# Kernel tuning notes

Measured on AMD Instinct MI355X. Metric: run time of the kernel, lower is better.

The kernel has to match this reference:

```python
import jax, jax.numpy as jnp
import numpy as np

V, D, T, H, L, NC = 50257, 1024, 512, 16, 4, 3
HS = D // H  # head size 64
DFF = 4 * D
B = 16


def _ln(x, g, b, eps=1e-5):
    mu = jnp.mean(x, axis=-1, keepdims=True)
    var = jnp.var(x, axis=-1, keepdims=True)
    return (x - mu) * jax.lax.rsqrt(var + eps) * g + b


def setup_inputs() -> dict:
    key = jax.random.key(0)
    ks = jax.random.split(key, 20)
    s = 0.02
    inp = {
        "x": jax.random.randint(ks[0], (B, T), 0, V),
        "tok_emb": jax.random.normal(ks[1], (V, D), jnp.float32) * s,
        "pos_emb": jax.random.normal(ks[2], (T, D), jnp.float32) * s,
        "Wq": jax.random.normal(ks[3], (L, H, D, HS), jnp.float32) * s,
        "Wk": jax.random.normal(ks[4], (L, H, D, HS), jnp.float32) * s,
        "Wv": jax.random.normal(ks[5], (L, H, D, HS), jnp.float32) * s,
        "Wproj": jax.random.normal(ks[6], (L, H * HS, D), jnp.float32) * s,
        "bproj": jnp.zeros((L, D), jnp.float32),
        "ln1_g": jnp.ones((L, D), jnp.float32),
        "ln1_b": jnp.zeros((L, D), jnp.float32),
        "ln2_g": jnp.ones((L, D), jnp.float32),
        "ln2_b": jnp.zeros((L, D), jnp.float32),
        "W1": jax.random.normal(ks[7], (L, D, DFF), jnp.float32) * s,
        "b1": jnp.zeros((L, DFF), jnp.float32),
        "W2": jax.random.normal(ks[8], (L, DFF, D), jnp.float32) * s,
        "b2": jnp.zeros((L, D), jnp.float32),
        "lnf_g": jnp.ones((D,), jnp.float32),
        "lnf_b": jnp.zeros((D,), jnp.float32),
        "Wout": jax.random.normal(ks[9], (T * D, NC), jnp.float32) * s,
        "bout": jnp.zeros((NC,), jnp.float32),
    }
    return inp


def reference(x, tok_emb, pos_emb, Wq, Wk, Wv, Wproj, bproj, ln1_g, ln1_b,
              ln2_g, ln2_b, W1, b1, W2, b2, lnf_g, lnf_b, Wout, bout):
    Bx, Tx = x.shape
    h = tok_emb[x] + pos_emb[:Tx]  # [B,T,D]; dropout=identity (eval)
    scale = HS ** -0.5
    for l in range(L):
        z = _ln(h, ln1_g[l], ln1_b[l])
        q = jnp.einsum('btd,hde->bhte', z, Wq[l])
        k = jnp.einsum('btd,hde->bhte', z, Wk[l])
        v = jnp.einsum('btd,hde->bhte', z, Wv[l])
        att = jax.nn.softmax(jnp.einsum('bhte,bhse->bhts', q, k) * scale, axis=-1)
        o = jnp.einsum('bhts,bhse->bhte', att, v)  # [B,H,T,HS]
        o = o.transpose(0, 2, 1, 3).reshape(Bx, Tx, H * HS)
        h = h + o @ Wproj[l] + bproj[l]
        z2 = _ln(h, ln2_g[l], ln2_b[l])
        ffn = jax.nn.gelu(z2 @ W1[l] + b1[l], approximate=False) @ W2[l] + b2[l]
        h = h + ffn
    h = _ln(h, lnf_g, lnf_b)
    logits = h.reshape(Bx, -1) @ Wout + bout  # [B,NC]
    return logits
```

## Files before the change

kernel.cpp:

```cpp
#include <hip/hip_runtime.h>
#include <math.h>
#include <stdint.h>

#define DEV __device__ __forceinline__

constexpr int Bz = 16, T = 512, D = 1024, H = 16, HS = 64, Lx = 4, DFF = 4096, NCn = 3;
constexpr int BT = Bz * T;

typedef __attribute__((ext_vector_type(8))) short v8s;
typedef __attribute__((ext_vector_type(4))) float v4f;

DEV uint16_t f2bf(float f) {
  uint32_t u = __float_as_uint(f);
  u += 0x7fff + ((u >> 16) & 1);
  return (uint16_t)(u >> 16);
}
DEV float bf2f(uint16_t v) { return __uint_as_float(((uint32_t)v) << 16); }

DEV void async_copy16(const void* g, void* l) {
  __builtin_amdgcn_global_load_lds(
      (const __attribute__((address_space(1))) uint32_t*)g,
      (__attribute__((address_space(3))) uint32_t*)l, 16, 0, 0);
}

__global__ void transpose_cast_kernel(const float* __restrict__ in, uint16_t* __restrict__ out,
                                      int R, int C) {
  __shared__ float tile[32][33];
  long bo = (long)blockIdx.z * R * C;
  in += bo; out += bo;
  int c0 = blockIdx.x * 32, r0 = blockIdx.y * 32;
  int tx = threadIdx.x, ty = threadIdx.y;
  for (int i = 0; i < 32; i += 8)
    tile[ty + i][tx] = in[(long)(r0 + ty + i) * C + (c0 + tx)];
  __syncthreads();
  for (int i = 0; i < 32; i += 8)
    out[(long)(c0 + ty + i) * R + (r0 + tx)] = f2bf(tile[tx][ty + i]);
}

__global__ void embed_kernel(const int* __restrict__ x, const float* __restrict__ tok,
                             const float* __restrict__ pos, float* __restrict__ h) {
  int row = blockIdx.x;
  int t = row & (T - 1);
  int id = x[row];
  const float4* tr = (const float4*)(tok + (long)id * D);
  const float4* pr = (const float4*)(pos + (long)t * D);
  float4* hr = (float4*)(h + (long)row * D);
  int i = threadIdx.x;
  float4 a = tr[i], b = pr[i];
  hr[i] = make_float4(a.x + b.x, a.y + b.y, a.z + b.z, a.w + b.w);
}

template <bool OUT_BF16>
__global__ void ln_kernel(const float* __restrict__ in, const float* __restrict__ g,
                          const float* __restrict__ b, void* __restrict__ out) {
  int row = blockIdx.x;
  int i = threadIdx.x;
  const float4* xr = (const float4*)(in + (long)row * D);
  float4 v = xr[i];
  float s = v.x + v.y + v.z + v.w;
  float s2 = v.x * v.x + v.y * v.y + v.z * v.z + v.w * v.w;
  for (int off = 32; off; off >>= 1) { s += __shfl_down(s, off); s2 += __shfl_down(s2, off); }
  __shared__ float sh1[4], sh2[4];
  int wid = i >> 6, lane = i & 63;
  if (lane == 0) { sh1[wid] = s; sh2[wid] = s2; }
  __syncthreads();
  s = sh1[0] + sh1[1] + sh1[2] + sh1[3];
  s2 = sh2[0] + sh2[1] + sh2[2] + sh2[3];
  float mu = s * (1.0f / D);
  float rstd = rsqrtf(s2 * (1.0f / D) - mu * mu + 1e-5f);
  float4 gv = ((const float4*)g)[i];
  float4 bv = ((const float4*)b)[i];
  float o0 = (v.x - mu) * rstd * gv.x + bv.x;
  float o1 = (v.y - mu) * rstd * gv.y + bv.y;
  float o2 = (v.z - mu) * rstd * gv.z + bv.z;
  float o3 = (v.w - mu) * rstd * gv.w + bv.w;
  if constexpr (OUT_BF16) {
    uint16_t* orow = (uint16_t*)out + (long)row * D;
    orow[4 * i + 0] = f2bf(o0); orow[4 * i + 1] = f2bf(o1);
    orow[4 * i + 2] = f2bf(o2); orow[4 * i + 3] = f2bf(o3);
  } else {
    ((float4*)((float*)out + (long)row * D))[i] = make_float4(o0, o1, o2, o3);
  }
}

__global__ void softmax_kernel(uint16_t* __restrict__ S) {
  long row = blockIdx.x;
  uint32_t* r = (uint32_t*)(S + row * (long)T);
  int i = threadIdx.x;
  uint32_t u = r[i];
  float a = __uint_as_float(u << 16) * 0.125f;
  float b = __uint_as_float(u & 0xffff0000u) * 0.125f;
  float m = fmaxf(a, b);
  for (int off = 32; off; off >>= 1) m = fmaxf(m, __shfl_down(m, off));
  __shared__ float sh[4], sh2[4];
  int wid = i >> 6, lane = i & 63;
  if (lane == 0) sh[wid] = m;
  __syncthreads();
  m = fmaxf(fmaxf(sh[0], sh[1]), fmaxf(sh[2], sh[3]));
  float ea = expf(a - m), eb = expf(b - m);
  float s = ea + eb;
  for (int off = 32; off; off >>= 1) s += __shfl_down(s, off);
  if (lane == 0) sh2[wid] = s;
  __syncthreads();
  float inv = 1.0f / (sh2[0] + sh2[1] + sh2[2] + sh2[3]);
  r[i] = (uint32_t)f2bf(ea * inv) | ((uint32_t)f2bf(eb * inv) << 16);
}

enum { MQK = 0, MVT = 1, MBF = 2, MO = 3, MRES = 4, MGELU = 5 };

template <int BM, int BN, int WGM, int WGN, int MODE>
__global__ void gemm_kernel(const uint16_t* __restrict__ A, const uint16_t* __restrict__ Bt,
                            int M, int N, int K,
                            long strideA, long strideB, long strideC,
                            const float* __restrict__ bias, void* __restrict__ Cout) {
  constexpr int BK = 32;
  constexpr int WM = BM / WGM, WN = BN / WGN;
  constexpr int TM = WM / 16, TN = WN / 16;
  __shared__ __align__(16) uint16_t As[BM * BK];
  __shared__ __align__(16) uint16_t Bs[BN * BK];
  int batch = blockIdx.z;
  A += (long)batch * strideA;
  Bt += (long)batch * strideB;
  int bn0 = blockIdx.x * BN, bm0 = blockIdx.y * BM;
  int tid = threadIdx.x, wid = tid >> 6, lane = tid & 63;
  int wm = wid / WGN, wn = wid % WGN;
  v4f acc[TM][TN] = {};
  const int laneRow = lane >> 2;
  const int laneB = (lane & 3) * 16;

  for (int k0 = 0; k0 < K; k0 += BK) {
    __syncthreads();
    for (int c = wid; c < BM / 16; c += 4) {
      int row = bm0 + c * 16 + laneRow;
      const char* g = (const char*)(A + (long)row * K + k0) + laneB;
      async_copy16(g, (char*)As + c * 1024);
    }
    for (int c = wid; c < BN / 16; c += 4) {
      int col = bn0 + c * 16 + laneRow;
      const char* g = (const char*)(Bt + (long)col * K + k0) + laneB;
      async_copy16(g, (char*)Bs + c * 1024);
    }
    __syncthreads();

    int kq = (lane >> 4) * 8;
    v8s af[TM], bfr[TN];
#pragma unroll
    for (int i = 0; i < TM; i++) {
      int r = wm * WM + i * 16 + (lane & 15);
      af[i] = *(const v8s*)&As[r * BK + kq];
    }
#pragma unroll
    for (int j = 0; j < TN; j++) {
      int c = wn * WN + j * 16 + (lane & 15);
      bfr[j] = *(const v8s*)&Bs[c * BK + kq];
    }
#pragma unroll
    for (int i = 0; i < TM; i++)
#pragma unroll
      for (int j = 0; j < TN; j++)
        acc[i][j] = __builtin_amdgcn_mfma_f32_16x16x32_bf16(af[i], bfr[j], acc[i][j], 0, 0, 0);
  }

#pragma unroll
  for (int i = 0; i < TM; i++) {
    int row0 = bm0 + wm * WM + i * 16 + (lane >> 4) * 4;
#pragma unroll
    for (int j = 0; j < TN; j++) {
      int col = bn0 + wn * WN + j * 16 + (lane & 15);
#pragma unroll
      for (int r = 0; r < 4; r++) {
        int row = row0 + r;
        float val = acc[i][j][r];
        if constexpr (MODE == MQK) {
          int b = row >> 9, t = row & 511, hh = col >> 6, e = col & 63;
          ((uint16_t*)Cout)[((long)(b * H + hh) * T + t) * HS + e] = f2bf(val);
        } else if constexpr (MODE == MVT) {
          int b = row >> 9, t = row & 511, hh = col >> 6, e = col & 63;
          ((uint16_t*)Cout)[((long)(b * H + hh) * HS + e) * T + t] = f2bf(val);
        } else if constexpr (MODE == MBF) {
          ((uint16_t*)Cout)[(long)batch * strideC + (long)row * N + col] = f2bf(val);
        } else if constexpr (MODE == MO) {
          int b = batch >> 4, hh = batch & 15;
          ((uint16_t*)Cout)[((long)(b * T + row) * H + hh) * HS + col] = f2bf(val);
        } else if constexpr (MODE == MRES) {
          ((float*)Cout)[(long)row * N + col] += val + bias[col];
        } else if constexpr (MODE == MGELU) {
          float xg = val + bias[col];
          float gl = 0.5f * xg * (1.0f + erff(xg * 0.70710678118f));
          ((uint16_t*)Cout)[(long)row * N + col] = f2bf(gl);
        }
      }
    }
  }
}

__global__ void logits_init(const float* __restrict__ bout, float* __restrict__ out) {
  int i = threadIdx.x;
  if (i < Bz * NCn) out[i] = bout[i % NCn];
}
__global__ void logits_kernel(const float* __restrict__ hf, const float* __restrict__ Wout,
                              float* __restrict__ out) {
  int b = blockIdx.y, c = blockIdx.z;
  long base = (long)blockIdx.x * 8192;
  const float* hv = hf + (long)b * T * D + base;
  const float* w = Wout + base * NCn + c;
  float s = 0.f;
  for (int i = threadIdx.x; i < 8192; i += 256) s += hv[i] * w[(long)i * NCn];
  for (int off = 32; off; off >>= 1) s += __shfl_down(s, off);
  __shared__ float sh[4];
  int wid = threadIdx.x >> 6, lane = threadIdx.x & 63;
  if (lane == 0) sh[wid] = s;
  __syncthreads();
  if (threadIdx.x == 0) atomicAdd(out + b * NCn + c, sh[0] + sh[1] + sh[2] + sh[3]);
}

extern "C" void kernel_launch(void* const* d_in, const int* in_sizes, int n_in,
                              void* d_out, int out_size, void* d_ws, size_t ws_size,
                              hipStream_t stream) {
  const int* x = (const int*)d_in[0];
  const float* tok = (const float*)d_in[1];
  const float* pos = (const float*)d_in[2];
  const float* Wq = (const float*)d_in[3];
  const float* Wk = (const float*)d_in[4];
  const float* Wv = (const float*)d_in[5];
  const float* Wproj = (const float*)d_in[6];
  const float* bproj = (const float*)d_in[7];
  const float* ln1g = (const float*)d_in[8];
  const float* ln1b = (const float*)d_in[9];
  const float* ln2g = (const float*)d_in[10];
  const float* ln2b = (const float*)d_in[11];
  const float* W1 = (const float*)d_in[12];
  const float* b1 = (const float*)d_in[13];
  const float* W2 = (const float*)d_in[14];
  const float* b2 = (const float*)d_in[15];
  const float* lnfg = (const float*)d_in[16];
  const float* lnfb = (const float*)d_in[17];
  const float* Wout = (const float*)d_in[18];
  const float* bout = (const float*)d_in[19];
  float* out = (float*)d_out;

  char* ws = (char*)d_ws;
  size_t off = 0;
  auto alloc = [&](size_t bytes) { char* p = ws + off; off += (bytes + 255) & ~(size_t)255; return p; };
  uint16_t* wqT = (uint16_t*)alloc((size_t)Lx * D * D * 2);
  uint16_t* wkT = (uint16_t*)alloc((size_t)Lx * D * D * 2);
  uint16_t* wvT = (uint16_t*)alloc((size_t)Lx * D * D * 2);
  uint16_t* wpT = (uint16_t*)alloc((size_t)Lx * D * D * 2);
  uint16_t* w1T = (uint16_t*)alloc((size_t)Lx * D * DFF * 2);
  uint16_t* w2T = (uint16_t*)alloc((size_t)Lx * D * DFF * 2);
  float* h = (float*)alloc((size_t)BT * D * 4);
  uint16_t* z = (uint16_t*)alloc((size_t)BT * D * 2);
  uint16_t* q = (uint16_t*)alloc((size_t)Bz * H * T * HS * 2);
  uint16_t* kb = (uint16_t*)alloc((size_t)Bz * H * T * HS * 2);
  uint16_t* vt = (uint16_t*)alloc((size_t)Bz * H * T * HS * 2);
  uint16_t* S = (uint16_t*)alloc((size_t)Bz * H * T * T * 2);
  uint16_t* o = (uint16_t*)alloc((size_t)BT * D * 2);
  uint16_t* a1 = (uint16_t*)alloc((size_t)BT * DFF * 2);
  (void)ws_size; (void)in_sizes; (void)n_in; (void)out_size;

  dim3 tb(32, 8);
  transpose_cast_kernel<<<dim3(HS / 32, D / 32, Lx * H), tb, 0, stream>>>(Wq, wqT, D, HS);
  transpose_cast_kernel<<<dim3(HS / 32, D / 32, Lx * H), tb, 0, stream>>>(Wk, wkT, D, HS);
  transpose_cast_kernel<<<dim3(HS / 32, D / 32, Lx * H), tb, 0, stream>>>(Wv, wvT, D, HS);
  transpose_cast_kernel<<<dim3(D / 32, D / 32, Lx), tb, 0, stream>>>(Wproj, wpT, D, D);
  transpose_cast_kernel<<<dim3(DFF / 32, D / 32, Lx), tb, 0, stream>>>(W1, w1T, D, DFF);
  transpose_cast_kernel<<<dim3(D / 32, DFF / 32, Lx), tb, 0, stream>>>(W2, w2T, DFF, D);

  embed_kernel<<<BT, 256, 0, stream>>>(x, tok, pos, h);

  for (int l = 0; l < Lx; l++) {
    const uint16_t* wq_l = wqT + (size_t)l * D * D;
    const uint16_t* wk_l = wkT + (size_t)l * D * D;
    const uint16_t* wv_l = wvT + (size_t)l * D * D;
    const uint16_t* wp_l = wpT + (size_t)l * D * D;
    const uint16_t* w1_l = w1T + (size_t)l * D * DFF;
    const uint16_t* w2_l = w2T + (size_t)l * D * DFF;

    ln_kernel<true><<<BT, 256, 0, stream>>>(h, ln1g + l * D, ln1b + l * D, z);

    gemm_kernel<128, 128, 2, 2, MQK><<<dim3(D / 128, BT / 128, 1), 256, 0, stream>>>(
        z, wq_l, BT, D, D, 0, 0, 0, nullptr, q);
    gemm_kernel<128, 128, 2, 2, MQK><<<dim3(D / 128, BT / 128, 1), 256, 0, stream>>>(
        z, wk_l, BT, D, D, 0, 0, 0, nullptr, kb);
    gemm_kernel<128, 128, 2, 2, MVT><<<dim3(D / 128, BT / 128, 1), 256, 0, stream>>>(
        z, wv_l, BT, D, D, 0, 0, 0, nullptr, vt);

    gemm_kernel<128, 128, 2, 2, MBF><<<dim3(T / 128, T / 128, Bz * H), 256, 0, stream>>>(
        q, kb, T, T, HS, (long)T * HS, (long)T * HS, (long)T * T, nullptr, S);

    softmax_kernel<<<(long)Bz * H * T, 256, 0, stream>>>(S);

    gemm_kernel<128, 64, 4, 1, MO><<<dim3(1, T / 128, Bz * H), 256, 0, stream>>>(
        S, vt, T, HS, T, (long)T * T, (long)HS * T, 0, nullptr, o);

    gemm_kernel<128, 128, 2, 2, MRES><<<dim3(D / 128, BT / 128, 1), 256, 0, stream>>>(
        o, wp_l, BT, D, D, 0, 0, 0, bproj + l * D, h);

    ln_kernel<true><<<BT, 256, 0, stream>>>(h, ln2g + l * D, ln2b + l * D, z);

    gemm_kernel<128, 128, 2, 2, MGELU><<<dim3(DFF / 128, BT / 128, 1), 256, 0, stream>>>(
        z, w1_l, BT, DFF, D, 0, 0, 0, b1 + l * DFF, a1);

    gemm_kernel<128, 128, 2, 2, MRES><<<dim3(D / 128, BT / 128, 1), 256, 0, stream>>>(
        a1, w2_l, BT, D, DFF, 0, 0, 0, b2 + l * D, h);
  }

  ln_kernel<false><<<BT, 256, 0, stream>>>(h, lnfg, lnfb, h);
  logits_init<<<1, 64, 0, stream>>>(bout, out);
  logits_kernel<<<dim3(64, Bz, NCn), 256, 0, stream>>>(h, Wout, out);
}
```

Baseline: 2.904 ms.

## Fuse QKV GEMM, swizzle LDS tiles, split-K atomics, warp-per-row softmax

Packs the Q, K and V weights into one transposed buffer so a single GEMM produces all three projections, removing two launches and rereads of the activations. An XOR swizzle is added to the LDS tile layout to reduce bank conflicts on fragment loads. The grid is reordered so blockIdx.x walks M. The residual GEMMs (projection and FFN2) are split along K into two halves that accumulate into h with atomicAdd, doubling block count at the cost of atomic traffic. Softmax is rewritten so each wavefront handles one row with 16-byte loads and shuffle reductions, dropping shared memory and block syncs.

```diff
diff --git a/kernel.cpp b/kernel.cpp
--- a/kernel.cpp
+++ b/kernel.cpp
@@ -6,6 +6,7 @@
 
 constexpr int Bz = 16, T = 512, D = 1024, H = 16, HS = 64, Lx = 4, DFF = 4096, NCn = 3;
 constexpr int BT = Bz * T;
+constexpr long QSZ = (long)Bz * H * T * HS;
 
 typedef __attribute__((ext_vector_type(8))) short v8s;
 typedef __attribute__((ext_vector_type(4))) float v4f;
@@ -15,7 +16,6 @@
   u += 0x7fff + ((u >> 16) & 1);
   return (uint16_t)(u >> 16);
 }
-DEV float bf2f(uint16_t v) { return __uint_as_float(((uint32_t)v) << 16); }
 
 DEV void async_copy16(const void* g, void* l) {
   __builtin_amdgcn_global_load_lds(
@@ -24,10 +24,11 @@
 }
 
 __global__ void transpose_cast_kernel(const float* __restrict__ in, uint16_t* __restrict__ out,
-                                      int R, int C) {
+                                      int R, int C, long s1, long s2, int zdiv) {
   __shared__ float tile[32][33];
-  long bo = (long)blockIdx.z * R * C;
-  in += bo; out += bo;
+  int zz = blockIdx.z;
+  in += (long)zz * R * C;
+  out += (long)(zz / zdiv) * s1 + (long)(zz % zdiv) * s2;
   int c0 = blockIdx.x * 32, r0 = blockIdx.y * 32;
   int tx = threadIdx.x, ty = threadIdx.y;
   for (int i = 0; i < 32; i += 8)
@@ -84,33 +85,41 @@
 }
 
 __global__ void softmax_kernel(uint16_t* __restrict__ S) {
-  long row = blockIdx.x;
-  uint32_t* r = (uint32_t*)(S + row * (long)T);
-  int i = threadIdx.x;
-  uint32_t u = r[i];
-  float a = __uint_as_float(u << 16) * 0.125f;
-  float b = __uint_as_float(u & 0xffff0000u) * 0.125f;
-  float m = fmaxf(a, b);
-  for (int off = 32; off; off >>= 1) m = fmaxf(m, __shfl_down(m, off));
-  __shared__ float sh[4], sh2[4];
-  int wid = i >> 6, lane = i & 63;
-  if (lane == 0) sh[wid] = m;
-  __syncthreads();
-  m = fmaxf(fmaxf(sh[0], sh[1]), fmaxf(sh[2], sh[3]));
-  float ea = expf(a - m), eb = expf(b - m);
-  float s = ea + eb;
-  for (int off = 32; off; off >>= 1) s += __shfl_down(s, off);
-  if (lane == 0) sh2[wid] = s;
-  __syncthreads();
-  float inv = 1.0f / (sh2[0] + sh2[1] + sh2[2] + sh2[3]);
-  r[i] = (uint32_t)f2bf(ea * inv) | ((uint32_t)f2bf(eb * inv) << 16);
-}
-
-enum { MQK = 0, MVT = 1, MBF = 2, MO = 3, MRES = 4, MGELU = 5 };
+  int wid = threadIdx.x >> 6, lane = threadIdx.x & 63;
+  long row = (long)blockIdx.x * 4 + wid;
+  uint4* p = (uint4*)(S + row * T) + lane;
+  uint4 u = *p;
+  uint32_t w[4] = {u.x, u.y, u.z, u.w};
+  float lo[4], hi[4];
+  float m = -1e30f;
+#pragma unroll
+  for (int i = 0; i < 4; i++) {
+    lo[i] = __uint_as_float(w[i] << 16) * 0.125f;
+    hi[i] = __uint_as_float(w[i] & 0xffff0000u) * 0.125f;
+    m = fmaxf(m, fmaxf(lo[i], hi[i]));
+  }
+  for (int off = 32; off; off >>= 1) m = fmaxf(m, __shfl_xor(m, off));
+  float s = 0.f;
+#pragma unroll
+  for (int i = 0; i < 4; i++) {
+    lo[i] = expf(lo[i] - m); hi[i] = expf(hi[i] - m);
+    s += lo[i] + hi[i];
+  }
+  for (int off = 32; off; off >>= 1) s += __shfl_xor(s, off);
+  float inv = 1.0f / s;
+  uint4 o;
+  uint32_t* ow = (uint32_t*)&o;
+#pragma unroll
+  for (int i = 0; i < 4; i++)
+    ow[i] = (uint32_t)f2bf(lo[i] * inv) | ((uint32_t)f2bf(hi[i] * inv) << 16);
+  *p = o;
+}
+
+enum { MQKV = 0, MBF = 1, MO = 2, MATOMIC = 3, MGELU = 4 };
 
 template <int BM, int BN, int WGM, int WGN, int MODE>
 __global__ void gemm_kernel(const uint16_t* __restrict__ A, const uint16_t* __restrict__ Bt,
-                            int M, int N, int K,
+                            int M, int N, int K, int lda, int ldb,
                             long strideA, long strideB, long strideC,
                             const float* __restrict__ bias, void* __restrict__ Cout) {
   constexpr int BK = 32;
@@ -118,42 +127,40 @@
   constexpr int TM = WM / 16, TN = WN / 16;
   __shared__ __align__(16) uint16_t As[BM * BK];
   __shared__ __align__(16) uint16_t Bs[BN * BK];
-  int batch = blockIdx.z;
+  int kz = 0, batch = 0;
+  if constexpr (MODE == MATOMIC) kz = blockIdx.z; else batch = blockIdx.z;
   A += (long)batch * strideA;
   Bt += (long)batch * strideB;
-  int bn0 = blockIdx.x * BN, bm0 = blockIdx.y * BM;
+  const int kb0 = kz * K;
+  int bm0 = blockIdx.x * BM, bn0 = blockIdx.y * BN;
   int tid = threadIdx.x, wid = tid >> 6, lane = tid & 63;
   int wm = wid / WGN, wn = wid % WGN;
   v4f acc[TM][TN] = {};
+
   const int laneRow = lane >> 2;
-  const int laneB = (lane & 3) * 16;
-
-  for (int k0 = 0; k0 < K; k0 += BK) {
+  const int laneB = ((lane & 3) ^ ((laneRow >> 1) & 3)) * 16;
+  const int rl = lane & 15;
+  const int cx16 = (rl * 4 + ((lane >> 4) ^ ((rl >> 1) & 3))) * 16;
+
+  for (int k0 = kb0; k0 < kb0 + K; k0 += BK) {
     __syncthreads();
     for (int c = wid; c < BM / 16; c += 4) {
       int row = bm0 + c * 16 + laneRow;
-      const char* g = (const char*)(A + (long)row * K + k0) + laneB;
-      async_copy16(g, (char*)As + c * 1024);
+      async_copy16((const char*)(A + (long)row * lda + k0) + laneB, (char*)As + c * 1024);
     }
     for (int c = wid; c < BN / 16; c += 4) {
       int col = bn0 + c * 16 + laneRow;
-      const char* g = (const char*)(Bt + (long)col * K + k0) + laneB;
-      async_copy16(g, (char*)Bs + c * 1024);
+      async_copy16((const char*)(Bt + (long)col * ldb + k0) + laneB, (char*)Bs + c * 1024);
     }
     __syncthreads();
 
-    int kq = (lane >> 4) * 8;
     v8s af[TM], bfr[TN];
 #pragma unroll
-    for (int i = 0; i < TM; i++) {
-      int r = wm * WM + i * 16 + (lane & 15);
-      af[i] = *(const v8s*)&As[r * BK + kq];
-    }
-#pragma unroll
-    for (int j = 0; j < TN; j++) {
-      int c = wn * WN + j * 16 + (lane & 15);
-      bfr[j] = *(const v8s*)&Bs[c * BK + kq];
-    }
+    for (int i = 0; i < TM; i++)
+      af[i] = *(const v8s*)((const char*)As + (wm * (WM / 16) + i) * 1024 + cx16);
+#pragma unroll
+    for (int j = 0; j < TN; j++)
+      bfr[j] = *(const v8s*)((const char*)Bs + (wn * (WN / 16) + j) * 1024 + cx16);
 #pragma unroll
     for (int i = 0; i < TM; i++)
 #pragma unroll
@@ -171,19 +178,21 @@
       for (int r = 0; r < 4; r++) {
         int row = row0 + r;
         float val = acc[i][j][r];
-        if constexpr (MODE == MQK) {
-          int b = row >> 9, t = row & 511, hh = col >> 6, e = col & 63;
-          ((uint16_t*)Cout)[((long)(b * H + hh) * T + t) * HS + e] = f2bf(val);
-        } else if constexpr (MODE == MVT) {
-          int b = row >> 9, t = row & 511, hh = col >> 6, e = col & 63;
-          ((uint16_t*)Cout)[((long)(b * H + hh) * HS + e) * T + t] = f2bf(val);
+        if constexpr (MODE == MQKV) {
+          int sel = col >> 10, c = col & 1023;
+          int hh = c >> 6, e = c & 63;
+          int b = row >> 9, t = row & 511;
+          long idx = (sel < 2) ? (((long)(b * H + hh) * T + t) * HS + e)
+                               : (((long)(b * H + hh) * HS + e) * T + t);
+          ((uint16_t*)Cout)[(long)sel * QSZ + idx] = f2bf(val);
         } else if constexpr (MODE == MBF) {
           ((uint16_t*)Cout)[(long)batch * strideC + (long)row * N + col] = f2bf(val);
         } else if constexpr (MODE == MO) {
           int b = batch >> 4, hh = batch & 15;
           ((uint16_t*)Cout)[((long)(b * T + row) * H + hh) * HS + col] = f2bf(val);
-        } else if constexpr (MODE == MRES) {
-          ((float*)Cout)[(long)row * N + col] += val + bias[col];
+        } else if constexpr (MODE == MATOMIC) {
+          float add = val + ((kz == 0) ? bias[col] : 0.f);
+          atomicAdd(&((float*)Cout)[(long)row * N + col], add);
         } else if constexpr (MODE == MGELU) {
           float xg = val + bias[col];
           float gl = 0.5f * xg * (1.0f + erff(xg * 0.70710678118f));
@@ -242,67 +251,67 @@
   char* ws = (char*)d_ws;
   size_t off = 0;
   auto alloc = [&](size_t bytes) { char* p = ws + off; off += (bytes + 255) & ~(size_t)255; return p; };
-  uint16_t* wqT = (uint16_t*)alloc((size_t)Lx * D * D * 2);
-  uint16_t* wkT = (uint16_t*)alloc((size_t)Lx * D * D * 2);
-  uint16_t* wvT = (uint16_t*)alloc((size_t)Lx * D * D * 2);
+  uint16_t* wqkvT = (uint16_t*)alloc((size_t)Lx * 3 * D * D * 2);
   uint16_t* wpT = (uint16_t*)alloc((size_t)Lx * D * D * 2);
   uint16_t* w1T = (uint16_t*)alloc((size_t)Lx * D * DFF * 2);
   uint16_t* w2T = (uint16_t*)alloc((size_t)Lx * D * DFF * 2);
   float* h = (float*)alloc((size_t)BT * D * 4);
   uint16_t* z = (uint16_t*)alloc((size_t)BT * D * 2);
-  uint16_t* q = (uint16_t*)alloc((size_t)Bz * H * T * HS * 2);
-  uint16_t* kb = (uint16_t*)alloc((size_t)Bz * H * T * HS * 2);
-  uint16_t* vt = (uint16_t*)alloc((size_t)Bz * H * T * HS * 2);
-  uint16_t* S = (uint16_t*)alloc((size_t)Bz * H * T * T * 2);
+  uint16_t* qkv = (uint16_t*)alloc((size_t)3 * QSZ * 2);
+  uint16_t* Sb = (uint16_t*)alloc((size_t)Bz * H * T * T * 2);
   uint16_t* o = (uint16_t*)alloc((size_t)BT * D * 2);
   uint16_t* a1 = (uint16_t*)alloc((size_t)BT * DFF * 2);
   (void)ws_size; (void)in_sizes; (void)n_in; (void)out_size;
 
+  uint16_t* q = qkv;
+  uint16_t* kb = qkv + QSZ;
+  uint16_t* vt = qkv + 2 * QSZ;
+
   dim3 tb(32, 8);
-  transpose_cast_kernel<<<dim3(HS / 32, D / 32, Lx * H), tb, 0, stream>>>(Wq, wqT, D, HS);
-  transpose_cast_kernel<<<dim3(HS / 32, D / 32, Lx * H), tb, 0, stream>>>(Wk, wkT, D, HS);
-  transpose_cast_kernel<<<dim3(HS / 32, D / 32, Lx * H), tb, 0, stream>>>(Wv, wvT, D, HS);
-  transpose_cast_kernel<<<dim3(D / 32, D / 32, Lx), tb, 0, stream>>>(Wproj, wpT, D, D);
-  transpose_cast_kernel<<<dim3(DFF / 32, D / 32, Lx), tb, 0, stream>>>(W1, w1T, D, DFF);
-  transpose_cast_kernel<<<dim3(D / 32, DFF / 32, Lx), tb, 0, stream>>>(W2, w2T, DFF, D);
+  transpose_cast_kernel<<<dim3(HS / 32, D / 32, Lx * H), tb, 0, stream>>>(
+      Wq, wqkvT, D, HS, 3L * D * D, (long)HS * D, H);
+  transpose_cast_kernel<<<dim3(HS / 32, D / 32, Lx * H), tb, 0, stream>>>(
+      Wk, wqkvT + (long)D * D, D, HS, 3L * D * D, (long)HS * D, H);
+  transpose_cast_kernel<<<dim3(HS / 32, D / 32, Lx * H), tb, 0, stream>>>(
+      Wv, wqkvT + 2L * D * D, D, HS, 3L * D * D, (long)HS * D, H);
+  transpose_cast_kernel<<<dim3(D / 32, D / 32, Lx), tb, 0, stream>>>(
+      Wproj, wpT, D, D, (long)D * D, 0, 1);
+  transpose_cast_kernel<<<dim3(DFF / 32, D / 32, Lx), tb, 0, stream>>>(
+      W1, w1T, D, DFF, (long)D * DFF, 0, 1);
+  transpose_cast_kernel<<<dim3(D / 32, DFF / 32, Lx), tb, 0, stream>>>(
+      W2, w2T, DFF, D, (long)D * DFF, 0, 1);
 
   embed_kernel<<<BT, 256, 0, stream>>>(x, tok, pos, h);
 
   for (int l = 0; l < Lx; l++) {
-    const uint16_t* wq_l = wqT + (size_t)l * D * D;
-    const uint16_t* wk_l = wkT + (size_t)l * D * D;
-    const uint16_t* wv_l = wvT + (size_t)l * D * D;
+    const uint16_t* wqkv_l = wqkvT + (size_t)l * 3 * D * D;
     const uint16_t* wp_l = wpT + (size_t)l * D * D;
     const uint16_t* w1_l = w1T + (size_t)l * D * DFF;
     const uint16_t* w2_l = w2T + (size_t)l * D * DFF;
 
     ln_kernel<true><<<BT, 256, 0, stream>>>(h, ln1g + l * D, ln1b + l * D, z);
 
-    gemm_kernel<128, 128, 2, 2, MQK><<<dim3(D / 128, BT / 128, 1), 256, 0, stream>>>(
-        z, wq_l, BT, D, D, 0, 0, 0, nullptr, q);
-    gemm_kernel<128, 128, 2, 2, MQK><<<dim3(D / 128, BT / 128, 1), 256, 0, stream>>>(
-        z, wk_l, BT, D, D, 0, 0, 0, nullptr, kb);
-    gemm_kernel<128, 128, 2, 2, MVT><<<dim3(D / 128, BT / 128, 1), 256, 0, stream>>>(
-        z, wv_l, BT, D, D, 0, 0, 0, nullptr, vt);
+    gemm_kernel<128, 128, 2, 2, MQKV><<<dim3(BT / 128, 3 * D / 128, 1), 256, 0, stream>>>(
+        z, wqkv_l, BT, 3 * D, D, D, D, 0, 0, 0, nullptr, qkv);
 
     gemm_kernel<128, 128, 2, 2, MBF><<<dim3(T / 128, T / 128, Bz * H), 256, 0, stream>>>(
-        q, kb, T, T, HS, (long)T * HS, (long)T * HS, (long)T * T, nullptr, S);
-
-    softmax_kernel<<<(long)Bz * H * T, 256, 0, stream>>>(S);
-
-    gemm_kernel<128, 64, 4, 1, MO><<<dim3(1, T / 128, Bz * H), 256, 0, stream>>>(
-        S, vt, T, HS, T, (long)T * T, (long)HS * T, 0, nullptr, o);
-
-    gemm_kernel<128, 128, 2, 2, MRES><<<dim3(D / 128, BT / 128, 1), 256, 0, stream>>>(
-        o, wp_l, BT, D, D, 0, 0, 0, bproj + l * D, h);
+        q, kb, T, T, HS, HS, HS, (long)T * HS, (long)T * HS, (long)T * T, nullptr, Sb);
+
+    softmax_kernel<<<Bz * H * T / 4, 256, 0, stream>>>(Sb);
+
+    gemm_kernel<128, 64, 4, 1, MO><<<dim3(T / 128, 1, Bz * H), 256, 0, stream>>>(
+        Sb, vt, T, HS, T, T, T, (long)T * T, (long)HS * T, 0, nullptr, o);
+
+    gemm_kernel<128, 128, 2, 2, MATOMIC><<<dim3(BT / 128, D / 128, 2), 256, 0, stream>>>(
+        o, wp_l, BT, D, D / 2, D, D, 0, 0, 0, bproj + l * D, h);
 
     ln_kernel<true><<<BT, 256, 0, stream>>>(h, ln2g + l * D, ln2b + l * D, z);
 
-    gemm_kernel<128, 128, 2, 2, MGELU><<<dim3(DFF / 128, BT / 128, 1), 256, 0, stream>>>(
-        z, w1_l, BT, DFF, D, 0, 0, 0, b1 + l * DFF, a1);
-
-    gemm_kernel<128, 128, 2, 2, MRES><<<dim3(D / 128, BT / 128, 1), 256, 0, stream>>>(
-        a1, w2_l, BT, D, DFF, 0, 0, 0, b2 + l * D, h);
+    gemm_kernel<128, 128, 2, 2, MGELU><<<dim3(BT / 128, DFF / 128, 1), 256, 0, stream>>>(
+        z, w1_l, BT, DFF, D, D, D, 0, 0, 0, b1 + l * DFF, a1);
+
+    gemm_kernel<128, 128, 2, 2, MATOMIC><<<dim3(BT / 128, D / 128, 2), 256, 0, stream>>>(
+        a1, w2_l, BT, D, DFF / 2, DFF, DFF, 0, 0, 0, b2 + l * D, h);
   }
 
   ln_kernel<false><<<BT, 256, 0, stream>>>(h, lnfg, lnfb, h);
```

Result: faster. 2.591 ms (-10.8%).
